# Kernel tuning notes

Hardware: AMD Instinct MI355X
Metric: run time of the kernel (lower is better)

## Reference

```python
import jax, jax.numpy as jnp
import numpy as np

M, N, D, B, LAYERS = 512, 512, 1024, 4096, 16


def setup_inputs() -> dict:
    key = jax.random.key(0)
    ks = jax.random.split(key, 4)
    x = jax.random.normal(ks[0], (M, B), dtype=jnp.float32)
    A = jax.random.normal(ks[1], (M, D), dtype=jnp.float32) / np.float32(np.sqrt(M))
    # fc[k].weight = A.t() + 0.001*randn  -> shape [d, m]
    W = A.T[None] + 0.001 * jax.random.normal(ks[2], (LAYERS, D, M), dtype=jnp.float32)
    Z0 = (1.0 / D) * jax.random.uniform(ks[3], (D, B), dtype=jnp.float32)
    E0 = jnp.zeros((M, B), dtype=jnp.float32)
    L0 = jnp.zeros((M, B), dtype=jnp.float32)
    ones = jnp.ones((LAYERS,), dtype=jnp.float32)
    return {
        'x': x, 'A': A, 'W': W, 'Z0': Z0, 'E0': E0, 'L0': L0,
        'beta1': ones, 'beta2': ones, 'beta3': ones, 'ss2': ones,
        'active_para': 0.2 * ones, 'active_para1': 0.8 * ones,
    }


def _soft(v, t):
    # self_active: relu(v - t) - relu(-v - t)  (soft threshold)
    return jax.nn.relu(v - t) - jax.nn.relu(-v - t)


def reference(x, A, W, Z0, E0, L0, beta1, beta2, beta3, ss2, active_para, active_para1):
    K = W.shape[0]
    # k = 0 (learned branch)
    T0 = A @ Z0 + E0 - x                      # [m, B]
    Var0 = L0 + beta1[0] * T0
    Z1 = _soft(Z0 - W[0] @ Var0, active_para[0])  # [d, B]

    def step(carry, params):
        Zp, Ep, Lp = carry
        b1, b2, b3, s2, ap, ap1, Wk = params
        AZ = A @ Zp                            # [m, B]
        VVar = Lp + b2 * (AZ + Ep - x)
        En = _soft(Ep - s2 * VVar, ap1)
        Tn = AZ + En - x
        Ln = Lp + b3 * Tn
        Varn = Ln + b1 * Tn
        Zn = _soft(Zp - Wk @ Varn, ap)
        return (Zn, En, Ln), (Zn, En, Ln)

    params = (beta1[1:], beta2[:K - 1], beta3[:K - 1], ss2[:K - 1],
              active_para[1:], active_para1[:K - 1], W[1:])
    _, (Zs, Es, Ls) = jax.lax.scan(step, (Z1, E0, L0), params)
    Z_all = jnp.concatenate([Z1[None], Zs], axis=0)   # [K, d, B]
    E_all = jnp.concatenate([E0[None], Es], axis=0)   # [K, m, B]
    L_all = jnp.concatenate([L0[None], Ls], axis=0)   # [K, m, B]
    return Z_all, E_all, L_all
```

## Files before the change

kernel.cpp:

```cpp
#include <hip/hip_runtime.h>
#include <cstddef>

#define MDIM 512
#define DDIM 1024
#define BDIM 4096
#define NLAYERS 16

constexpr int BK = 16;

__device__ __forceinline__ float softf(float v, float t) {
  return copysignf(fmaxf(fabsf(v) - t, 0.0f), v);
}

template <int MODE, int K>
__global__ __launch_bounds__(256) void gemm_bc(
    const float* __restrict__ P, const float* __restrict__ Bm,
    const float* __restrict__ xg, const float* __restrict__ Ep,
    const float* __restrict__ Lp, const float* __restrict__ Zp,
    const float* __restrict__ beta1, const float* __restrict__ beta2,
    const float* __restrict__ beta3, const float* __restrict__ ss2,
    const float* __restrict__ apar, const float* __restrict__ apar1, int k,
    float* __restrict__ O0, float* __restrict__ O1, float* __restrict__ O2) {
  __shared__ __align__(16) float As[2][BK][32];
  __shared__ __align__(16) float Bs[2][BK][128];

  const int tid = threadIdx.x;
  const int lane = tid & 63;
  const int w = __builtin_amdgcn_readfirstlane((int)(tid >> 6));
  const int m0 = blockIdx.x * 32, n0 = blockIdx.y * 128;
  const int r0 = m0 + w * 8;
  const int c0 = n0 + lane * 2;

  float acc[8][2];
#pragma unroll
  for (int r = 0; r < 8; ++r) {
    acc[r][0] = 0.0f;
    acc[r][1] = 0.0f;
  }

  const int ar = tid >> 3, akc = (tid & 7) * 2;
  const float* gA = P + (size_t)(m0 + ar) * K + akc;
  const int br = tid >> 4, bc = (tid & 15) * 8;
  const float* gB = Bm + (size_t)br * BDIM + n0 + bc;

  float2 rA;
  float4 rB0, rB1;
  auto gload = [&](int k0) {
    rA = *reinterpret_cast<const float2*>(gA + (size_t)k0);
    rB0 = *reinterpret_cast<const float4*>(gB + (size_t)k0 * BDIM);
    rB1 = *reinterpret_cast<const float4*>(gB + (size_t)k0 * BDIM + 4);
  };
  auto stagewr = [&](int bb) {
    As[bb][akc][ar] = rA.x;
    As[bb][akc + 1][ar] = rA.y;
    *reinterpret_cast<float4*>(&Bs[bb][br][bc]) = rB0;
    *reinterpret_cast<float4*>(&Bs[bb][br][bc + 4]) = rB1;
  };
  auto comp = [&](int bb) {
#pragma unroll
    for (int kk = 0; kk < BK; ++kk) {
      const float4 a0 = *reinterpret_cast<const float4*>(&As[bb][kk][w * 8]);
      const float4 a1 =
          *reinterpret_cast<const float4*>(&As[bb][kk][w * 8 + 4]);
      const float a[8] = {a0.x, a0.y, a0.z, a0.w, a1.x, a1.y, a1.z, a1.w};
      const float2 b2 = *reinterpret_cast<const float2*>(&Bs[bb][kk][lane * 2]);
#pragma unroll
      for (int r = 0; r < 8; ++r) {
        acc[r][0] = fmaf(a[r], b2.x, acc[r][0]);
        acc[r][1] = fmaf(a[r], b2.y, acc[r][1]);
      }
    }
  };

  constexpr int NS = K / BK;
  gload(0);
  stagewr(0);
  __syncthreads();
  int bb = 0;
#pragma unroll 1
  for (int t = 1; t < NS; ++t) {
    gload(t * BK);
    comp(bb);
    stagewr(bb ^ 1);
    __syncthreads();
    bb ^= 1;
  }
  comp(bb);

  const float b1v = (MODE == 2) ? 0.f : beta1[k];
  float b2v = 0.f, b3v = 0.f, s2v = 0.f, a1v = 0.f, ap = 0.f;
  if (MODE == 1) {
    b2v = beta2[k - 1];
    b3v = beta3[k - 1];
    s2v = ss2[k - 1];
    a1v = apar1[k - 1];
  }
  if (MODE == 2) ap = apar[k];

#pragma unroll
  for (int r = 0; r < 8; ++r) {
    const size_t off = (size_t)(r0 + r) * BDIM + c0;
    if (MODE == 2) {
      const float2 z2 = *reinterpret_cast<const float2*>(&Zp[off]);
      float2 o;
      o.x = softf(z2.x - acc[r][0], ap);
      o.y = softf(z2.y - acc[r][1], ap);
      *reinterpret_cast<float2*>(&O0[off]) = o;
    } else {
      const float2 e2 = *reinterpret_cast<const float2*>(&Ep[off]);
      const float2 l2 = *reinterpret_cast<const float2*>(&Lp[off]);
      const float2 x2 = *reinterpret_cast<const float2*>(&xg[off]);
      const float ev[2] = {e2.x, e2.y};
      const float lv[2] = {l2.x, l2.y};
      const float xv[2] = {x2.x, x2.y};
      float vo[2], eo[2], lo_[2];
#pragma unroll
      for (int j = 0; j < 2; ++j) {
        const float az = acc[r][j];
        if (MODE == 0) {
          const float t0 = az + ev[j] - xv[j];
          vo[j] = fmaf(b1v, t0, lv[j]);
          eo[j] = ev[j];
          lo_[j] = lv[j];
        } else {
          const float vv = fmaf(b2v, az + ev[j] - xv[j], lv[j]);
          const float en = softf(ev[j] - s2v * vv, a1v);
          const float tn_ = az + en - xv[j];
          const float ln = fmaf(b3v, tn_, lv[j]);
          eo[j] = en;
          lo_[j] = ln;
          vo[j] = fmaf(b1v, tn_, ln);
        }
      }
      float2 t2;
      t2.x = vo[0];
      t2.y = vo[1];
      *reinterpret_cast<float2*>(&O0[off]) = t2;
      t2.x = eo[0];
      t2.y = eo[1];
      *reinterpret_cast<float2*>(&O1[off]) = t2;
      t2.x = lo_[0];
      t2.y = lo_[1];
      *reinterpret_cast<float2*>(&O2[off]) = t2;
    }
  }
}

extern "C" void kernel_launch(void* const* d_in, const int* in_sizes, int n_in,
                              void* d_out, int out_size, void* d_ws,
                              size_t ws_size, hipStream_t stream) {
  (void)in_sizes;
  (void)n_in;
  (void)out_size;
  (void)ws_size;
  const float* x = (const float*)d_in[0];
  const float* A = (const float*)d_in[1];
  const float* W = (const float*)d_in[2];
  const float* Z0 = (const float*)d_in[3];
  const float* E0 = (const float*)d_in[4];
  const float* L0 = (const float*)d_in[5];
  const float* beta1 = (const float*)d_in[6];
  const float* beta2 = (const float*)d_in[7];
  const float* beta3 = (const float*)d_in[8];
  const float* ss2 = (const float*)d_in[9];
  const float* apar = (const float*)d_in[10];
  const float* apar1 = (const float*)d_in[11];

  constexpr size_t DB = (size_t)DDIM * BDIM;
  constexpr size_t MB = (size_t)MDIM * BDIM;
  float* Zall = (float*)d_out;
  float* Eall = Zall + (size_t)NLAYERS * DB;
  float* Lall = Eall + (size_t)NLAYERS * MB;
  float* Var = (float*)d_ws;

  const dim3 blk(256);
  const dim3 gA(MDIM / 32, BDIM / 128);
  const dim3 gB(DDIM / 32, BDIM / 128);

  gemm_bc<0, DDIM><<<gA, blk, 0, stream>>>(
      A, Z0, x, E0, L0, nullptr, beta1, beta2, beta3, ss2, apar, apar1, 0, Var,
      Eall, Lall);
  gemm_bc<2, MDIM><<<gB, blk, 0, stream>>>(
      W, Var, nullptr, nullptr, nullptr, Z0, beta1, beta2, beta3, ss2, apar,
      apar1, 0, Zall, nullptr, nullptr);
  for (int k = 1; k < NLAYERS; ++k) {
    const float* Zp = Zall + (size_t)(k - 1) * DB;
    gemm_bc<1, DDIM><<<gA, blk, 0, stream>>>(
        A, Zp, x, Eall + (size_t)(k - 1) * MB, Lall + (size_t)(k - 1) * MB,
        nullptr, beta1, beta2, beta3, ss2, apar, apar1, k, Var,
        Eall + (size_t)k * MB, Lall + (size_t)k * MB);
    gemm_bc<2, MDIM><<<gB, blk, 0, stream>>>(
        W + (size_t)k * DDIM * MDIM, Var, nullptr, nullptr, nullptr, Zp, beta1,
        beta2, beta3, ss2, apar, apar1, k, Zall + (size_t)k * DB, nullptr,
        nullptr);
  }
}
```

Before: 2.445 ms.

## Load A operand via wave-uniform scalar loads instead of LDS, widen K tile

The A-matrix tile is no longer staged through shared memory. Each wave reads its 8 rows directly from global memory with wave-uniform addresses, which the compiler can turn into scalar loads. The K tile grows from 16 to 32 and the B tile row is padded to 132 floats, with per-kernel launch-bound occupancy hints. The aim is to cut LDS traffic and synchronisation per FMA, at the cost of more registers (an 8x8 A block per sub-step) and exposed global-load latency on A.

Result: slower. 3.986 ms (+63.1%).

```diff
diff --git a/kernel.cpp b/kernel.cpp
--- a/kernel.cpp
+++ b/kernel.cpp
@@ -6,14 +6,15 @@
 #define BDIM 4096
 #define NLAYERS 16
 
-constexpr int BK = 16;
+constexpr int BK = 32;
+constexpr int BNP = 132;
 
 __device__ __forceinline__ float softf(float v, float t) {
   return copysignf(fmaxf(fabsf(v) - t, 0.0f), v);
 }
 
-template <int MODE, int K>
-__global__ __launch_bounds__(256) void gemm_bc(
+template <int MODE, int K, int MINW>
+__global__ __launch_bounds__(256, MINW) void gemm_sg(
     const float* __restrict__ P, const float* __restrict__ Bm,
     const float* __restrict__ xg, const float* __restrict__ Ep,
     const float* __restrict__ Lp, const float* __restrict__ Zp,
@@ -21,8 +22,7 @@
     const float* __restrict__ beta3, const float* __restrict__ ss2,
     const float* __restrict__ apar, const float* __restrict__ apar1, int k,
     float* __restrict__ O0, float* __restrict__ O1, float* __restrict__ O2) {
-  __shared__ __align__(16) float As[2][BK][32];
-  __shared__ __align__(16) float Bs[2][BK][128];
+  __shared__ __align__(16) float Bs[2][BK][BNP];
 
   const int tid = threadIdx.x;
   const int lane = tid & 63;
@@ -31,6 +31,8 @@
   const int r0 = m0 + w * 8;
   const int c0 = n0 + lane * 2;
 
+  const float* pA = P + (size_t)r0 * K;
+
   float acc[8][2];
 #pragma unroll
   for (int r = 0; r < 8; ++r) {
@@ -38,36 +40,39 @@
     acc[r][1] = 0.0f;
   }
 
-  const int ar = tid >> 3, akc = (tid & 7) * 2;
-  const float* gA = P + (size_t)(m0 + ar) * K + akc;
-  const int br = tid >> 4, bc = (tid & 15) * 8;
-  const float* gB = Bm + (size_t)br * BDIM + n0 + bc;
-
-  float2 rA;
-  float4 rB0, rB1;
+  const int srow = tid >> 3, scol = (tid & 7) * 16;
+  const float* gB = Bm + (size_t)srow * BDIM + n0 + scol;
+
+  float4 rb[4];
   auto gload = [&](int k0) {
-    rA = *reinterpret_cast<const float2*>(gA + (size_t)k0);
-    rB0 = *reinterpret_cast<const float4*>(gB + (size_t)k0 * BDIM);
-    rB1 = *reinterpret_cast<const float4*>(gB + (size_t)k0 * BDIM + 4);
+#pragma unroll
+    for (int j = 0; j < 4; ++j)
+      rb[j] = *reinterpret_cast<const float4*>(gB + (size_t)k0 * BDIM + j * 4);
   };
   auto stagewr = [&](int bb) {
-    As[bb][akc][ar] = rA.x;
-    As[bb][akc + 1][ar] = rA.y;
-    *reinterpret_cast<float4*>(&Bs[bb][br][bc]) = rB0;
-    *reinterpret_cast<float4*>(&Bs[bb][br][bc + 4]) = rB1;
+#pragma unroll
+    for (int j = 0; j < 4; ++j)
+      *reinterpret_cast<float4*>(&Bs[bb][srow][scol + j * 4]) = rb[j];
   };
-  auto comp = [&](int bb) {
-#pragma unroll
-    for (int kk = 0; kk < BK; ++kk) {
-      const float4 a0 = *reinterpret_cast<const float4*>(&As[bb][kk][w * 8]);
-      const float4 a1 =
-          *reinterpret_cast<const float4*>(&As[bb][kk][w * 8 + 4]);
-      const float a[8] = {a0.x, a0.y, a0.z, a0.w, a1.x, a1.y, a1.z, a1.w};
-      const float2 b2 = *reinterpret_cast<const float2*>(&Bs[bb][kk][lane * 2]);
-#pragma unroll
-      for (int r = 0; r < 8; ++r) {
-        acc[r][0] = fmaf(a[r], b2.x, acc[r][0]);
-        acc[r][1] = fmaf(a[r], b2.y, acc[r][1]);
+  auto comp = [&](int bb, int k0) {
+#pragma unroll
+    for (int s = 0; s < 4; ++s) {
+      float a[8][8];
+#pragma unroll
+      for (int r = 0; r < 8; ++r)
+#pragma unroll
+        for (int q = 0; q < 8; ++q)
+          a[r][q] = pA[(size_t)r * K + k0 + s * 8 + q];
+#pragma unroll
+      for (int q = 0; q < 8; ++q) {
+        const int kk = s * 8 + q;
+        const float2 b2 =
+            *reinterpret_cast<const float2*>(&Bs[bb][kk][lane * 2]);
+#pragma unroll
+        for (int r = 0; r < 8; ++r) {
+          acc[r][0] = fmaf(a[r][q], b2.x, acc[r][0]);
+          acc[r][1] = fmaf(a[r][q], b2.y, acc[r][1]);
+        }
       }
     }
   };
@@ -80,12 +85,12 @@
 #pragma unroll 1
   for (int t = 1; t < NS; ++t) {
     gload(t * BK);
-    comp(bb);
+    comp(bb, (t - 1) * BK);
     stagewr(bb ^ 1);
     __syncthreads();
     bb ^= 1;
   }
-  comp(bb);
+  comp(bb, (NS - 1) * BK);
 
   const float b1v = (MODE == 2) ? 0.f : beta1[k];
   float b2v = 0.f, b3v = 0.f, s2v = 0.f, a1v = 0.f, ap = 0.f;
@@ -177,19 +182,19 @@
   const dim3 gA(MDIM / 32, BDIM / 128);
   const dim3 gB(DDIM / 32, BDIM / 128);
 
-  gemm_bc<0, DDIM><<<gA, blk, 0, stream>>>(
+  gemm_sg<0, DDIM, 2><<<gA, blk, 0, stream>>>(
       A, Z0, x, E0, L0, nullptr, beta1, beta2, beta3, ss2, apar, apar1, 0, Var,
       Eall, Lall);
-  gemm_bc<2, MDIM><<<gB, blk, 0, stream>>>(
+  gemm_sg<2, MDIM, 4><<<gB, blk, 0, stream>>>(
       W, Var, nullptr, nullptr, nullptr, Z0, beta1, beta2, beta3, ss2, apar,
       apar1, 0, Zall, nullptr, nullptr);
   for (int k = 1; k < NLAYERS; ++k) {
     const float* Zp = Zall + (size_t)(k - 1) * DB;
-    gemm_bc<1, DDIM><<<gA, blk, 0, stream>>>(
+    gemm_sg<1, DDIM, 2><<<gA, blk, 0, stream>>>(
         A, Zp, x, Eall + (size_t)(k - 1) * MB, Lall + (size_t)(k - 1) * MB,
         nullptr, beta1, beta2, beta3, ss2, apar, apar1, k, Var,
         Eall + (size_t)k * MB, Lall + (size_t)k * MB);
-    gemm_bc<2, MDIM><<<gB, blk, 0, stream>>>(
+    gemm_sg<2, MDIM, 4><<<gB, blk, 0, stream>>>(
         W + (size_t)k * DDIM * MDIM, Var, nullptr, nullptr, nullptr, Zp, beta1,
         beta2, beta3, ss2, apar, apar1, k, Zall + (size_t)k * DB, nullptr,
         nullptr);
```
